# Kernel tuning notes

Hardware: AMD Instinct MI355X
Metric: run time of the kernel (lower is better)

## Reference

```python
import jax, jax.numpy as jnp
import numpy as np

B, D, H = 524288, 64, 19  # batch, input_size, hidden_size


def setup_inputs() -> dict:
    key = jax.random.key(0)
    ks = jax.random.split(key, 4)
    x = jax.random.normal(ks[0], (B, D), dtype=jnp.float32)
    # nn.Linear params (stored as [out, in] like torch)
    Wi = jax.random.normal(ks[1], (H, D), dtype=jnp.float32) / np.sqrt(D).astype(np.float32)
    bi = jnp.zeros((H,), jnp.float32)
    Wr = jax.random.normal(ks[2], (H, H), dtype=jnp.float32) / np.sqrt(H).astype(np.float32)
    Wo = jax.random.normal(ks[3], (H, H), dtype=jnp.float32) / np.sqrt(H).astype(np.float32)
    bo = jnp.zeros((H,), jnp.float32)
    tau = jnp.full((H,), 0.5, jnp.float32)        # nn.Parameter(ones*0.5)
    tau_adapt = jnp.full((H,), 0.1, jnp.float32)  # nn.Parameter(ones*0.1)
    return {"x": x, "Wi": Wi, "bi": bi, "Wr": Wr, "Wo": Wo, "bo": bo,
            "tau": tau, "tau_adapt": tau_adapt, "steps": 10}


def reference(x, Wi, bi, Wr, Wo, bo, tau, tau_adapt, steps):
    dt = 0.01
    # scalar urgency over the whole input, clamped from below
    urgency = jnp.maximum(jnp.abs(x).mean(), 0.01)
    tau_dyn = jnp.clip(tau * (1.0 - tau_adapt) + tau_adapt / urgency, 0.01, 10.0)  # [H]
    mapped = x @ Wi.T + bi  # [B, H], computed once outside the loop
    h0 = jnp.zeros((x.shape[0], tau.shape[0]), x.dtype)

    def step(h, _):
        act = jnp.tanh(mapped + h @ Wr.T)
        h = h + dt * ((-h + act) / tau_dyn)
        return h, None

    h, _ = jax.lax.scan(step, h0, None, length=steps)
    return (h @ Wo.T + bo, h)
```

## Files before the change

kernel.cpp:

```cpp
#include <hip/hip_runtime.h>

#define NB 524288
#define ND 64
#define NH 19
#define NP 10
#define NBLK_A 8192

typedef float v2f __attribute__((ext_vector_type(2)));

__device__ __forceinline__ v2f splat2(float x) { return (v2f){x, x}; }
__device__ __forceinline__ v2f fma2(v2f a, v2f b, v2f c) {
    return __builtin_elementwise_fma(a, b, c);
}

__device__ __forceinline__ v2f tanh2(v2f x) {
    v2f x2 = x * x;
    v2f n  = fma2(x2, x2 + splat2(105.f), splat2(945.f));
    v2f d  = fma2(x2, fma2(x2, splat2(15.f), splat2(420.f)), splat2(945.f));
    v2f xn = x * n;
    v2f y  = {xn.x * __builtin_amdgcn_rcpf(d.x), xn.y * __builtin_amdgcn_rcpf(d.y)};
    y = __builtin_elementwise_min(y, splat2(1.f));
    y = __builtin_elementwise_max(y, splat2(-1.f));
    return y;
}

extern "C" __global__ void __launch_bounds__(64)
ltc_setup(const float* __restrict__ Wr, const float* __restrict__ Wo,
          const float* __restrict__ bo, float2* __restrict__ Wr2,
          float2* __restrict__ Wo2, float2* __restrict__ bo2)
{
    for (int i = threadIdx.x; i < NH * NP; i += 64) {
        int k = i / NP, t = i % NP;
        float rx = Wr[(2 * t) * NH + k];
        float ry = (2 * t + 1 < NH) ? Wr[(2 * t + 1) * NH + k] : 0.f;
        Wr2[i] = make_float2(rx, ry);
        float ox = Wo[(2 * t) * NH + k];
        float oy = (2 * t + 1 < NH) ? Wo[(2 * t + 1) * NH + k] : 0.f;
        Wo2[i] = make_float2(ox, oy);
    }
    if (threadIdx.x < NP) {
        int t = threadIdx.x;
        bo2[t] = make_float2(bo[2 * t], (2 * t + 1 < NH) ? bo[2 * t + 1] : 0.f);
    }
}

extern "C" __global__ void __launch_bounds__(64)
ltc_a(const float* __restrict__ x, const float* __restrict__ Wi,
      const float* __restrict__ bi, float* __restrict__ mapped,
      float* __restrict__ partials)
{
    __shared__ float tile[64 * 66];
    const int l = threadIdx.x;
    const int rowbase = blockIdx.x * 64;
    const float4* xg = (const float4*)x + (size_t)rowbase * (ND / 4);
    float s = 0.f;
#pragma unroll
    for (int i = 0; i < 16; ++i) {
        const float4 v = xg[i * 64 + l];
        s += fabsf(v.x) + fabsf(v.y) + fabsf(v.z) + fabsf(v.w);
        const int f = i * 64 + l, row = f >> 4, c = f & 15;
        *(float2*)&tile[row * 66 + c * 4]     = make_float2(v.x, v.y);
        *(float2*)&tile[row * 66 + c * 4 + 2] = make_float2(v.z, v.w);
    }
    __syncthreads();
    float m[NH];
#pragma unroll
    for (int j = 0; j < NH; ++j) m[j] = bi[j];
#pragma unroll
    for (int q = 0; q < ND / 2; ++q) {
        const float2 v = *(const float2*)&tile[l * 66 + 2 * q];
#pragma unroll
        for (int j = 0; j < NH; ++j) {
            m[j] = fmaf(v.x, Wi[j * ND + 2 * q], m[j]);
            m[j] = fmaf(v.y, Wi[j * ND + 2 * q + 1], m[j]);
        }
    }
#pragma unroll
    for (int j = 0; j < NH; ++j) mapped[(size_t)j * NB + rowbase + l] = m[j];
#pragma unroll
    for (int off = 32; off > 0; off >>= 1) s += __shfl_down(s, off, 64);
    if (l == 0) partials[blockIdx.x] = s;
}

extern "C" __global__ void __launch_bounds__(256)
ltc_b(const float* __restrict__ mapped, const float* __restrict__ partials,
      const float2* __restrict__ Wr2, const float2* __restrict__ Wo2,
      const float2* __restrict__ bo2, const float* __restrict__ tau,
      const float* __restrict__ ta, const int* __restrict__ steps_p,
      float* __restrict__ out)
{
    __shared__ float st[256 * NH];
    __shared__ float red[4];
    const int t = threadIdx.x;
    const int b = blockIdx.x * 256 + t;

    float ps = 0.f;
#pragma unroll
    for (int i = 0; i < NBLK_A / 256; ++i) ps += partials[t + 256 * i];
#pragma unroll
    for (int off = 32; off > 0; off >>= 1) ps += __shfl_down(ps, off, 64);
    if ((t & 63) == 0) red[t >> 6] = ps;
    __syncthreads();
    const float total = red[0] + red[1] + red[2] + red[3];
    const float u = fmaxf(total * (1.f / ((float)NB * (float)ND)), 0.01f);
    const float inv_u = 1.f / u;

    v2f rr2[NP];
#pragma unroll
    for (int j = 0; j < NP; ++j) {
        int j0 = 2 * j, j1 = (2 * j + 1 < NH) ? 2 * j + 1 : 2 * j;
        float t0 = fminf(10.f, fmaxf(0.01f, tau[j0] * (1.f - ta[j0]) + ta[j0] * inv_u));
        float t1 = fminf(10.f, fmaxf(0.01f, tau[j1] * (1.f - ta[j1]) + ta[j1] * inv_u));
        rr2[j] = (v2f){0.01f / t0, 0.01f / t1};
    }

    v2f m2[NP], h2[NP];
#pragma unroll
    for (int j = 0; j < NP - 1; ++j)
        m2[j] = (v2f){mapped[(size_t)(2 * j) * NB + b],
                      mapped[(size_t)(2 * j + 1) * NB + b]};
    m2[NP - 1] = (v2f){mapped[(size_t)(NH - 1) * NB + b], 0.f};
#pragma unroll
    for (int j = 0; j < NP; ++j) h2[j] = splat2(0.f);

    const int steps = *steps_p;
    const v2f* wr = (const v2f*)Wr2;
    for (int s = 0; s < steps; ++s) {
        v2f p2[NP];
        {
            const v2f hb = splat2(h2[0].x);
#pragma unroll
            for (int j = 0; j < NP; ++j) p2[j] = fma2(hb, wr[j], m2[j]);
        }
#pragma unroll
        for (int k = 1; k < NH; ++k) {
            const float hk = (k & 1) ? h2[k >> 1].y : h2[k >> 1].x;
            const v2f hb = splat2(hk);
            const v2f* wrow = wr + k * NP;
#pragma unroll
            for (int j = 0; j < NP; ++j) p2[j] = fma2(hb, wrow[j], p2[j]);
        }
#pragma unroll
        for (int j = 0; j < NP; ++j) p2[j] = tanh2(p2[j]);
#pragma unroll
        for (int j = 0; j < NP; ++j) h2[j] = fma2(rr2[j], p2[j] - h2[j], h2[j]);
    }

    const v2f* wo = (const v2f*)Wo2;
    v2f o2[NP];
    {
        const v2f hb = splat2(h2[0].x);
        const v2f* bb = (const v2f*)bo2;
#pragma unroll
        for (int j = 0; j < NP; ++j) o2[j] = fma2(hb, wo[j], bb[j]);
    }
#pragma unroll
    for (int k = 1; k < NH; ++k) {
        const float hk = (k & 1) ? h2[k >> 1].y : h2[k >> 1].x;
        const v2f hb = splat2(hk);
        const v2f* worow = wo + k * NP;
#pragma unroll
        for (int j = 0; j < NP; ++j) o2[j] = fma2(hb, worow[j], o2[j]);
    }
    __syncthreads();
#pragma unroll
    for (int j = 0; j < NH; ++j)
        st[t * NH + j] = (j & 1) ? o2[j >> 1].y : o2[j >> 1].x;
    __syncthreads();
    {
        const float4* s4 = (const float4*)st;
        float4* o4 = (float4*)(out + (size_t)blockIdx.x * 256 * NH);
#pragma unroll
        for (int i = 0; i < 4; ++i) o4[t + i * 256] = s4[t + i * 256];
        if (t + 1024 < 1216) o4[t + 1024] = s4[t + 1024];
    }
    __syncthreads();
#pragma unroll
    for (int j = 0; j < NH; ++j)
        st[t * NH + j] = (j & 1) ? h2[j >> 1].y : h2[j >> 1].x;
    __syncthreads();
    {
        const float4* s4 = (const float4*)st;
        float4* o4 = (float4*)(out + (size_t)NB * NH + (size_t)blockIdx.x * 256 * NH);
#pragma unroll
        for (int i = 0; i < 4; ++i) o4[t + i * 256] = s4[t + i * 256];
        if (t + 1024 < 1216) o4[t + 1024] = s4[t + 1024];
    }
}

extern "C" void kernel_launch(void* const* d_in, const int* in_sizes, int n_in,
                              void* d_out, int out_size, void* d_ws, size_t ws_size,
                              hipStream_t stream)
{
    const float* x   = (const float*)d_in[0];
    const float* Wi  = (const float*)d_in[1];
    const float* bi  = (const float*)d_in[2];
    const float* Wr  = (const float*)d_in[3];
    const float* Wo  = (const float*)d_in[4];
    const float* bo  = (const float*)d_in[5];
    const float* tau = (const float*)d_in[6];
    const float* ta  = (const float*)d_in[7];
    const int* steps = (const int*)d_in[8];
    float* out = (float*)d_out;

    float*  partials = (float*)d_ws;
    float2* Wr2 = (float2*)((char*)d_ws + 32768);
    float2* Wo2 = (float2*)((char*)d_ws + 34304);
    float2* bo2 = (float2*)((char*)d_ws + 35840);
    float*  mapped = (float*)((char*)d_ws + 36864);

    ltc_setup<<<1, 64, 0, stream>>>(Wr, Wo, bo, Wr2, Wo2, bo2);
    ltc_a<<<NBLK_A, 64, 0, stream>>>(x, Wi, bi, mapped, partials);
    ltc_b<<<NB / 256, 256, 0, stream>>>(mapped, partials, Wr2, Wo2, bo2,
                                        tau, ta, steps, out);
}
```

Before: 358.6 us.

## Fuse input projection into recurrence kernel and split abs-sum into separate pass

The input projection x@Wi.T moves from its own kernel into the recurrence kernel, so the [B,H] mapped intermediate is no longer written to and read back from global memory. A lightweight abs-sum kernel computes the urgency partials first, which means x is now read twice (once for the sum, once for the projection). Wi is repacked into float2 pairs so the projection uses packed FMAs, and the urgency scalar is made wave-uniform with readfirstlane. The fused kernel uses more LDS and registers, which could lower occupancy.

Result: slower. 372.5 us (+3.9%).

```diff
diff --git a/kernel.cpp b/kernel.cpp
--- a/kernel.cpp
+++ b/kernel.cpp
@@ -4,13 +4,18 @@
 #define ND 64
 #define NH 19
 #define NP 10
-#define NBLK_A 8192
+#define NBLK 2048
 
 typedef float v2f __attribute__((ext_vector_type(2)));
 
 __device__ __forceinline__ v2f splat2(float x) { return (v2f){x, x}; }
 __device__ __forceinline__ v2f fma2(v2f a, v2f b, v2f c) {
     return __builtin_elementwise_fma(a, b, c);
+}
+__device__ __forceinline__ float rfl(float v) {
+    union { float f; int i; } a; a.f = v;
+    a.i = __builtin_amdgcn_readfirstlane(a.i);
+    return a.f;
 }
 
 __device__ __forceinline__ v2f tanh2(v2f x) {
@@ -25,9 +30,12 @@
 }
 
 extern "C" __global__ void __launch_bounds__(64)
-ltc_setup(const float* __restrict__ Wr, const float* __restrict__ Wo,
-          const float* __restrict__ bo, float2* __restrict__ Wr2,
-          float2* __restrict__ Wo2, float2* __restrict__ bo2)
+ltc_setup(const float* __restrict__ Wi, const float* __restrict__ bi,
+          const float* __restrict__ Wr, const float* __restrict__ Wo,
+          const float* __restrict__ bo,
+          float2* __restrict__ Wi2, float2* __restrict__ bi2,
+          float2* __restrict__ Wr2, float2* __restrict__ Wo2,
+          float2* __restrict__ bo2)
 {
     for (int i = threadIdx.x; i < NH * NP; i += 64) {
         int k = i / NP, t = i % NP;
@@ -38,72 +46,94 @@
         float oy = (2 * t + 1 < NH) ? Wo[(2 * t + 1) * NH + k] : 0.f;
         Wo2[i] = make_float2(ox, oy);
     }
+    for (int i = threadIdx.x; i < ND * NP; i += 64) {
+        int col = i / NP, t = i % NP;
+        float ax = Wi[(2 * t) * ND + col];
+        float ay = (2 * t + 1 < NH) ? Wi[(2 * t + 1) * ND + col] : 0.f;
+        Wi2[i] = make_float2(ax, ay);
+    }
     if (threadIdx.x < NP) {
         int t = threadIdx.x;
         bo2[t] = make_float2(bo[2 * t], (2 * t + 1 < NH) ? bo[2 * t + 1] : 0.f);
-    }
-}
-
-extern "C" __global__ void __launch_bounds__(64)
-ltc_a(const float* __restrict__ x, const float* __restrict__ Wi,
-      const float* __restrict__ bi, float* __restrict__ mapped,
-      float* __restrict__ partials)
-{
-    __shared__ float tile[64 * 66];
-    const int l = threadIdx.x;
-    const int rowbase = blockIdx.x * 64;
-    const float4* xg = (const float4*)x + (size_t)rowbase * (ND / 4);
-    float s = 0.f;
-#pragma unroll
-    for (int i = 0; i < 16; ++i) {
-        const float4 v = xg[i * 64 + l];
-        s += fabsf(v.x) + fabsf(v.y) + fabsf(v.z) + fabsf(v.w);
-        const int f = i * 64 + l, row = f >> 4, c = f & 15;
-        *(float2*)&tile[row * 66 + c * 4]     = make_float2(v.x, v.y);
-        *(float2*)&tile[row * 66 + c * 4 + 2] = make_float2(v.z, v.w);
-    }
-    __syncthreads();
-    float m[NH];
-#pragma unroll
-    for (int j = 0; j < NH; ++j) m[j] = bi[j];
-#pragma unroll
-    for (int q = 0; q < ND / 2; ++q) {
-        const float2 v = *(const float2*)&tile[l * 66 + 2 * q];
-#pragma unroll
-        for (int j = 0; j < NH; ++j) {
-            m[j] = fmaf(v.x, Wi[j * ND + 2 * q], m[j]);
-            m[j] = fmaf(v.y, Wi[j * ND + 2 * q + 1], m[j]);
-        }
-    }
-#pragma unroll
-    for (int j = 0; j < NH; ++j) mapped[(size_t)j * NB + rowbase + l] = m[j];
-#pragma unroll
-    for (int off = 32; off > 0; off >>= 1) s += __shfl_down(s, off, 64);
-    if (l == 0) partials[blockIdx.x] = s;
+        bi2[t] = make_float2(bi[2 * t], (2 * t + 1 < NH) ? bi[2 * t + 1] : 0.f);
+    }
 }
 
 extern "C" __global__ void __launch_bounds__(256)
-ltc_b(const float* __restrict__ mapped, const float* __restrict__ partials,
-      const float2* __restrict__ Wr2, const float2* __restrict__ Wo2,
-      const float2* __restrict__ bo2, const float* __restrict__ tau,
-      const float* __restrict__ ta, const int* __restrict__ steps_p,
-      float* __restrict__ out)
-{
-    __shared__ float st[256 * NH];
+ltc_absum(const float* __restrict__ x, float* __restrict__ partials)
+{
     __shared__ float red[4];
     const int t = threadIdx.x;
-    const int b = blockIdx.x * 256 + t;
+    const float4* xg = (const float4*)x + (size_t)blockIdx.x * 4096;
+    float s = 0.f;
+#pragma unroll
+    for (int i = 0; i < 16; ++i) {
+        const float4 v = xg[i * 256 + t];
+        s += fabsf(v.x) + fabsf(v.y) + fabsf(v.z) + fabsf(v.w);
+    }
+#pragma unroll
+    for (int off = 32; off > 0; off >>= 1) s += __shfl_down(s, off, 64);
+    if ((t & 63) == 0) red[t >> 6] = s;
+    __syncthreads();
+    if (t == 0) partials[blockIdx.x] = red[0] + red[1] + red[2] + red[3];
+}
+
+extern "C" __global__ void __launch_bounds__(256, 4)
+ltc_fused(const float* __restrict__ x, const float* __restrict__ partials,
+          const v2f* __restrict__ Wi2, const v2f* __restrict__ bi2,
+          const v2f* __restrict__ Wr2, const v2f* __restrict__ Wo2,
+          const v2f* __restrict__ bo2, const float* __restrict__ tau,
+          const float* __restrict__ ta, const int* __restrict__ steps_p,
+          float* __restrict__ out)
+{
+    __shared__ float lds[4 * 64 * 34];
+    __shared__ float red[4];
+    const int t = threadIdx.x;
+    const int l = t & 63, w = t >> 6;
+    const int rowbase = blockIdx.x * 256;
 
     float ps = 0.f;
 #pragma unroll
-    for (int i = 0; i < NBLK_A / 256; ++i) ps += partials[t + 256 * i];
+    for (int i = 0; i < NBLK / 256; ++i) ps += partials[t + 256 * i];
 #pragma unroll
     for (int off = 32; off > 0; off >>= 1) ps += __shfl_down(ps, off, 64);
     if ((t & 63) == 0) red[t >> 6] = ps;
     __syncthreads();
     const float total = red[0] + red[1] + red[2] + red[3];
-    const float u = fmaxf(total * (1.f / ((float)NB * (float)ND)), 0.01f);
+    const float u = rfl(fmaxf(total * (1.f / ((float)NB * (float)ND)), 0.01f));
     const float inv_u = 1.f / u;
+
+    v2f m2[NP];
+#pragma unroll
+    for (int j = 0; j < NP; ++j) m2[j] = bi2[j];
+    {
+        float* tw = lds + w * (64 * 34);
+        const float4* xg = (const float4*)x + (size_t)(rowbase + w * 64) * 16;
+#pragma unroll
+        for (int c = 0; c < 2; ++c) {
+#pragma unroll
+            for (int i = 0; i < 8; ++i) {
+                const int flat = i * 64 + l, row = flat >> 3, cq = flat & 7;
+                const float4 v = xg[row * 16 + c * 8 + cq];
+                *(float2*)&tw[row * 34 + cq * 4]     = make_float2(v.x, v.y);
+                *(float2*)&tw[row * 34 + cq * 4 + 2] = make_float2(v.z, v.w);
+            }
+            __syncthreads();
+#pragma unroll
+            for (int q = 0; q < 16; ++q) {
+                const float2 v = *(const float2*)&tw[l * 34 + 2 * q];
+                const int col = c * 32 + 2 * q;
+                const v2f vx = splat2(v.x), vy = splat2(v.y);
+                const v2f* wc0 = Wi2 + (size_t)col * NP;
+                const v2f* wc1 = Wi2 + (size_t)(col + 1) * NP;
+#pragma unroll
+                for (int j = 0; j < NP; ++j) m2[j] = fma2(vx, wc0[j], m2[j]);
+#pragma unroll
+                for (int j = 0; j < NP; ++j) m2[j] = fma2(vy, wc1[j], m2[j]);
+            }
+            __syncthreads();
+        }
+    }
 
     v2f rr2[NP];
 #pragma unroll
@@ -114,17 +144,12 @@
         rr2[j] = (v2f){0.01f / t0, 0.01f / t1};
     }
 
-    v2f m2[NP], h2[NP];
-#pragma unroll
-    for (int j = 0; j < NP - 1; ++j)
-        m2[j] = (v2f){mapped[(size_t)(2 * j) * NB + b],
-                      mapped[(size_t)(2 * j + 1) * NB + b]};
-    m2[NP - 1] = (v2f){mapped[(size_t)(NH - 1) * NB + b], 0.f};
+    v2f h2[NP];
 #pragma unroll
     for (int j = 0; j < NP; ++j) h2[j] = splat2(0.f);
 
     const int steps = *steps_p;
-    const v2f* wr = (const v2f*)Wr2;
+    const v2f* wr = Wr2;
     for (int s = 0; s < steps; ++s) {
         v2f p2[NP];
         {
@@ -146,13 +171,12 @@
         for (int j = 0; j < NP; ++j) h2[j] = fma2(rr2[j], p2[j] - h2[j], h2[j]);
     }
 
-    const v2f* wo = (const v2f*)Wo2;
+    const v2f* wo = Wo2;
     v2f o2[NP];
     {
         const v2f hb = splat2(h2[0].x);
-        const v2f* bb = (const v2f*)bo2;
-#pragma unroll
-        for (int j = 0; j < NP; ++j) o2[j] = fma2(hb, wo[j], bb[j]);
+#pragma unroll
+        for (int j = 0; j < NP; ++j) o2[j] = fma2(hb, wo[j], bo2[j]);
     }
 #pragma unroll
     for (int k = 1; k < NH; ++k) {
@@ -162,6 +186,7 @@
 #pragma unroll
         for (int j = 0; j < NP; ++j) o2[j] = fma2(hb, worow[j], o2[j]);
     }
+    float* st = lds;
     __syncthreads();
 #pragma unroll
     for (int j = 0; j < NH; ++j)
@@ -204,13 +229,16 @@
     float* out = (float*)d_out;
 
     float*  partials = (float*)d_ws;
-    float2* Wr2 = (float2*)((char*)d_ws + 32768);
-    float2* Wo2 = (float2*)((char*)d_ws + 34304);
-    float2* bo2 = (float2*)((char*)d_ws + 35840);
-    float*  mapped = (float*)((char*)d_ws + 36864);
-
-    ltc_setup<<<1, 64, 0, stream>>>(Wr, Wo, bo, Wr2, Wo2, bo2);
-    ltc_a<<<NBLK_A, 64, 0, stream>>>(x, Wi, bi, mapped, partials);
-    ltc_b<<<NB / 256, 256, 0, stream>>>(mapped, partials, Wr2, Wo2, bo2,
+    float2* Wr2 = (float2*)((char*)d_ws + 8192);
+    float2* Wo2 = (float2*)((char*)d_ws + 9728);
+    float2* bo2 = (float2*)((char*)d_ws + 11264);
+    float2* bi2 = (float2*)((char*)d_ws + 11360);
+    float2* Wi2 = (float2*)((char*)d_ws + 11456);
+
+    ltc_setup<<<1, 64, 0, stream>>>(Wi, bi, Wr, Wo, bo, Wi2, bi2, Wr2, Wo2, bo2);
+    ltc_absum<<<NBLK, 256, 0, stream>>>(x, partials);
+    ltc_fused<<<NBLK, 256, 0, stream>>>(x, partials, (const v2f*)Wi2,
+                                        (const v2f*)bi2, (const v2f*)Wr2,
+                                        (const v2f*)Wo2, (const v2f*)bo2,
                                         tau, ta, steps, out);
 }
```
